# Optimization experiments

Hardware: AMD Instinct MI355X
Metric: run time of the kernel (lower is better)

The kernel has to match this reference:

```python
import jax, jax.numpy as jnp
import numpy as np

N_NODES = 50000
N_EDGES = 600000
IN_DIM, HID, OUT_DIM = 128, 128, 64
LN_EPS = 1e-5


def setup_inputs() -> dict:
    key = jax.random.key(0)
    ks = jax.random.split(key, 10)
    def glorot(k, shape):
        lim = np.sqrt(6.0 / (shape[0] + shape[1]))
        return jax.random.uniform(k, shape, jnp.float32, -lim, lim)
    return {
        "x": jax.random.normal(ks[0], (N_NODES, IN_DIM), jnp.float32),
        "src": jax.random.randint(ks[1], (N_EDGES,), 0, N_NODES, jnp.int32),
        "dst": jax.random.randint(ks[2], (N_EDGES,), 0, N_NODES, jnp.int32),
        "W0": glorot(ks[3], (IN_DIM, HID)), "b0": jnp.zeros((HID,), jnp.float32),
        "W1": glorot(ks[4], (HID, HID)),    "b1": jnp.zeros((HID,), jnp.float32),
        "W2": glorot(ks[5], (HID, OUT_DIM)),"b2": jnp.zeros((OUT_DIM,), jnp.float32),
        "ln_scale": jnp.ones((HID,), jnp.float32),
        "ln_bias": jnp.zeros((HID,), jnp.float32),
    }


def _degree_norms(src, dst):
    ones = jnp.ones((src.shape[0],), jnp.float32)
    deg_out = jax.ops.segment_sum(ones, src, num_segments=N_NODES)
    deg_in = jax.ops.segment_sum(ones, dst, num_segments=N_NODES)
    # DGL clamps degree to min 1 for norm='both'
    out_norm = jnp.clip(deg_out, 1.0, None) ** -0.5
    in_norm = jnp.clip(deg_in, 1.0, None) ** -0.5
    return out_norm, in_norm


def _graph_conv(h, src, dst, out_norm, in_norm, W, b):
    # norm='both': scale src side, SpMM aggregate, scale dst side, then affine
    h = h * out_norm[:, None]
    h = h @ W  # apply weight first (mathematically identical, smaller messages when out<in)
    agg = jax.ops.segment_sum(h[src], dst, num_segments=N_NODES)  # [N, D]
    return agg * in_norm[:, None] + b


def _layernorm(h, scale, bias):
    mu = jnp.mean(h, axis=-1, keepdims=True)
    var = jnp.var(h, axis=-1, keepdims=True)
    return (h - mu) * jax.lax.rsqrt(var + LN_EPS) * scale + bias


def reference(x, src, dst, W0, b0, W1, b1, W2, b2, ln_scale, ln_bias):
    out_norm, in_norm = _degree_norms(src, dst)
    # dropout is identity in eval mode
    h = jax.nn.relu(_graph_conv(x, src, dst, out_norm, in_norm, W0, b0))
    h = _layernorm(h, ln_scale, ln_bias)
    h = jax.nn.relu(_graph_conv(h, src, dst, out_norm, in_norm, W1, b1))
    h = _layernorm(h, ln_scale, ln_bias)
    # last layer: encoding=True -> keep activation; no norm after last layer
    h = jax.nn.relu(_graph_conv(h, src, dst, out_norm, in_norm, W2, b2))
    return h
```

## Files before the change

kernel.cpp:

```cpp
#include <hip/hip_runtime.h>
#include <hip/hip_fp16.h>

#define NN 50000
#define NE 600000
#define LN_EPS 1e-5f
#define SCAN_B 49
#define RANGES 8
#define RSZ 6250
#define CHUNKS 30
#define CSZ 20000

typedef __attribute__((ext_vector_type(8))) _Float16 half8;
typedef __attribute__((ext_vector_type(4))) float floatx4;

__device__ __align__(16) __half g_h0[NN * 128];
__device__ __align__(16) __half g_h1[NN * 128];
__device__ float g_out_norm[NN];
__device__ float g_in_norm[NN];
__device__ int g_rowptr[NN + 1];
__device__ int g_esrc[NE];
__device__ int g_blocksum[SCAN_B];
__device__ int g_perm[NN];
__device__ int g_dhist[SCAN_B * 256];
__device__ int g_pout[CHUNKS * NN];
__device__ int g_pin[CHUNKS * NN];
__device__ int g_base[CHUNKS * NN];
__device__ unsigned g_bar_count = 0;
__device__ unsigned g_bar_gen = 0;

__device__ __forceinline__ __half* hbuf(int i) { return i ? g_h1 : g_h0; }

__device__ __forceinline__ void gridbar(unsigned* expected) {
    __syncthreads();
    if (threadIdx.x == 0) {
        __threadfence();
        unsigned prev = __hip_atomic_fetch_add(&g_bar_count, 1u, __ATOMIC_ACQ_REL,
                                               __HIP_MEMORY_SCOPE_AGENT);
        if (prev == gridDim.x - 1) {
            __hip_atomic_store(&g_bar_count, 0u, __ATOMIC_RELAXED, __HIP_MEMORY_SCOPE_AGENT);
            __hip_atomic_fetch_add(&g_bar_gen, 1u, __ATOMIC_RELEASE, __HIP_MEMORY_SCOPE_AGENT);
        } else {
            while (__hip_atomic_load(&g_bar_gen, __ATOMIC_ACQUIRE, __HIP_MEMORY_SCOPE_AGENT) ==
                   *expected)
                __builtin_amdgcn_s_sleep(8);
        }
        __threadfence();
    }
    __syncthreads();
    (*expected)++;
}

__global__ __launch_bounds__(256) void histo_kernel(const int* __restrict__ src,
                                                    const int* __restrict__ dst) {
    __shared__ int h_out[RSZ];
    __shared__ int h_in[RSZ];
    int c = blockIdx.x / RANGES, r = blockIdx.x % RANGES;
    int lo = r * RSZ;
    for (int i = threadIdx.x; i < RSZ; i += 256) { h_out[i] = 0; h_in[i] = 0; }
    __syncthreads();
    const int4* s4 = (const int4*)(src + c * CSZ);
    const int4* d4 = (const int4*)(dst + c * CSZ);
    for (int i = threadIdx.x; i < CSZ / 4; i += 256) {
        int4 s = s4[i], d = d4[i];
        int v;
        v = s.x - lo; if ((unsigned)v < RSZ) atomicAdd(&h_out[v], 1);
        v = s.y - lo; if ((unsigned)v < RSZ) atomicAdd(&h_out[v], 1);
        v = s.z - lo; if ((unsigned)v < RSZ) atomicAdd(&h_out[v], 1);
        v = s.w - lo; if ((unsigned)v < RSZ) atomicAdd(&h_out[v], 1);
        v = d.x - lo; if ((unsigned)v < RSZ) atomicAdd(&h_in[v], 1);
        v = d.y - lo; if ((unsigned)v < RSZ) atomicAdd(&h_in[v], 1);
        v = d.z - lo; if ((unsigned)v < RSZ) atomicAdd(&h_in[v], 1);
        v = d.w - lo; if ((unsigned)v < RSZ) atomicAdd(&h_in[v], 1);
    }
    __syncthreads();
    for (int i = threadIdx.x; i < RSZ; i += 256) {
        g_pout[c * NN + lo + i] = h_out[i];
        g_pin[c * NN + lo + i]  = h_in[i];
    }
}

__global__ __launch_bounds__(1024) void mid_kernel() {
    __shared__ int sums[1024];
    __shared__ int aux[64];
    __shared__ int hist[256];
    __shared__ int cursor[256];
    unsigned expected = __hip_atomic_load(&g_bar_gen, __ATOMIC_RELAXED, __HIP_MEMORY_SCOPE_AGENT);
    int b = blockIdx.x, t = threadIdx.x;
    int n = b * 1024 + t;
    if (t < 256) hist[t] = 0;
    int si = 0;
    if (n < NN) {
        int so = 0;
#pragma unroll
        for (int c = 0; c < CHUNKS; ++c) { so += g_pout[c * NN + n]; si += g_pin[c * NN + n]; }
        g_out_norm[n] = rsqrtf((float)max(so, 1));
        g_in_norm[n]  = rsqrtf((float)max(si, 1));
    }
    __syncthreads();
    int bin = min(si, 255);
    if (n < NN) atomicAdd(&hist[bin], 1);
    int s = si;
#pragma unroll
    for (int off = 32; off; off >>= 1) s += __shfl_xor(s, off, 64);
    if ((t & 63) == 0) aux[t >> 6] = s;
    __syncthreads();
    if (t < 256) g_dhist[b * 256 + t] = hist[t];
    if (t < 16) {
        int v = aux[t];
#pragma unroll
        for (int off = 8; off; off >>= 1) v += __shfl_xor(v, off, 16);
        if (t == 0) g_blocksum[b] = v;
    }
    gridbar(&expected);
    if (t < 64) {
        int own = (t < SCAN_B) ? g_blocksum[t] : 0;
        int v = own;
#pragma unroll
        for (int off = 1; off < 64; off <<= 1) {
            int nb = __shfl_up(v, off, 64);
            if (t >= off) v += nb;
        }
        aux[t] = v - own;
        if (b == 0 && t == SCAN_B - 1) g_rowptr[NN] = v;
    }
    __syncthreads();
    int blockoff = aux[b];
    sums[t] = si;
    __syncthreads();
    for (int off = 1; off < 1024; off <<= 1) {
        int add = (t >= off) ? sums[t - off] : 0;
        __syncthreads();
        sums[t] += add;
        __syncthreads();
    }
    int excl = sums[t] - si + blockoff;
    if (n < NN) {
        g_rowptr[n] = excl;
        int run = excl;
#pragma unroll
        for (int c = 0; c < CHUNKS; ++c) {
            g_base[c * NN + n] = run;
            run += g_pin[c * NN + n];
        }
    }
    int cur = 0, tot = 0;
    if (t < 256) {
        for (int b2 = 0; b2 < SCAN_B; ++b2) {
            int h = g_dhist[b2 * 256 + t];
            if (b2 < b) cur += h;
            tot += h;
        }
        cursor[t] = tot;
    }
    __syncthreads();
    for (int off = 1; off < 256; off <<= 1) {
        int add = (t < 256 && t >= off) ? cursor[t - off] : 0;
        __syncthreads();
        if (t < 256) cursor[t] += add;
        __syncthreads();
    }
    if (t < 256) cursor[t] = cursor[t] - tot + cur;
    __syncthreads();
    if (n < NN) {
        int pos = atomicAdd(&cursor[bin], 1);
        g_perm[pos] = n;
    }
}

__global__ __launch_bounds__(256) void place_lds_kernel(const int* __restrict__ src,
                                                        const int* __restrict__ dst) {
    __shared__ int cur[RSZ];
    int c = blockIdx.x / RANGES, r = blockIdx.x % RANGES;
    int lo = r * RSZ;
    for (int i = threadIdx.x; i < RSZ; i += 256) cur[i] = g_base[c * NN + lo + i];
    __syncthreads();
    const int4* s4 = (const int4*)(src + c * CSZ);
    const int4* d4 = (const int4*)(dst + c * CSZ);
    for (int i = threadIdx.x; i < CSZ / 4; i += 256) {
        int4 s = s4[i], d = d4[i];
        int v, p;
        v = d.x - lo; if ((unsigned)v < RSZ) { p = atomicAdd(&cur[v], 1); g_esrc[p] = s.x; }
        v = d.y - lo; if ((unsigned)v < RSZ) { p = atomicAdd(&cur[v], 1); g_esrc[p] = s.y; }
        v = d.z - lo; if ((unsigned)v < RSZ) { p = atomicAdd(&cur[v], 1); g_esrc[p] = s.z; }
        v = d.w - lo; if ((unsigned)v < RSZ) { p = atomicAdd(&cur[v], 1); g_esrc[p] = s.w; }
    }
}

template <int N, bool AEXT>
__global__ __launch_bounds__(256) void gemm_mfma(const float* __restrict__ Aext,
                                                 int a_ib, int c_ib,
                                                 const float* __restrict__ Wg,
                                                 int M) {
    constexpr int NT = N / 16;
    constexpr int LOGN = (N == 128) ? 7 : 6;
    __shared__ _Float16 Wl[128 * N];

    const int tid = threadIdx.x;
    for (int e = tid; e < 128 * N; e += 256) {
        int k = e >> LOGN, n = e & (N - 1);
        Wl[(((k >> 3) * N + n) << 3) + (k & 7)] = (_Float16)Wg[e];
    }
    __syncthreads();

    const int wv = tid >> 6, lane = tid & 63;
    const int quad = lane >> 4, mrow = lane & 15;
    const int rowbase = blockIdx.x * 64 + wv * 16;
    const int arow0 = rowbase + mrow;
    const int arow = (arow0 < M) ? arow0 : (M - 1);

    floatx4 acc[NT] = {};
    const __half* Ah = AEXT ? nullptr : hbuf(a_ib);

#pragma unroll
    for (int kk = 0; kk < 4; ++kk) {
        const int k0 = kk * 32 + quad * 8;
        half8 afrag;
        if (AEXT) {
            const float4* ap = (const float4*)(Aext + (size_t)arow * 128 + k0);
            float4 f0 = ap[0], f1 = ap[1];
            afrag[0] = (_Float16)f0.x; afrag[1] = (_Float16)f0.y;
            afrag[2] = (_Float16)f0.z; afrag[3] = (_Float16)f0.w;
            afrag[4] = (_Float16)f1.x; afrag[5] = (_Float16)f1.y;
            afrag[6] = (_Float16)f1.z; afrag[7] = (_Float16)f1.w;
        } else {
            afrag = *(const half8*)(Ah + (size_t)arow * 128 + k0);
        }
#pragma unroll
        for (int nt = 0; nt < NT; ++nt) {
            half8 bfrag = *(const half8*)&Wl[(((kk * 4 + quad) * N + nt * 16 + mrow) << 3)];
            acc[nt] = __builtin_amdgcn_mfma_f32_16x16x32_f16(afrag, bfrag, acc[nt], 0, 0, 0);
        }
    }

    __half* C = hbuf(c_ib);
#pragma unroll
    for (int r = 0; r < 4; ++r) {
        int crow = rowbase + quad * 4 + r;
        if (crow < M) {
            float s = g_out_norm[crow];
#pragma unroll
            for (int nt = 0; nt < NT; ++nt) {
                float v = acc[nt][r] * s;
                C[(size_t)crow * N + nt * 16 + mrow] = __float2half_rn(v);
            }
        }
    }
}

#define ACC8(u) { \
    float2 f0 = __half22float2(*(const __half2*)&(u).x); \
    float2 f1 = __half22float2(*(const __half2*)&(u).y); \
    float2 f2 = __half22float2(*(const __half2*)&(u).z); \
    float2 f3 = __half22float2(*(const __half2*)&(u).w); \
    a0 += f0.x; a1 += f0.y; a2 += f1.x; a3 += f1.y; \
    a4 += f2.x; a5 += f2.y; a6 += f3.x; a7 += f3.y; }

__global__ __launch_bounds__(256) void gather_ln_kernel(int s_ib, int d_ib,
                                                        const float* __restrict__ b,
                                                        const float* __restrict__ ln_s,
                                                        const float* __restrict__ ln_b) {
    int wave = threadIdx.x >> 6;
    int lane = threadIdx.x & 63;
    int sub = lane >> 4, sl = lane & 15;
    int idx = blockIdx.x * 16 + wave * 4 + sub;
    int node = g_perm[idx];
    const uint4* Hu = (const uint4*)hbuf(s_ib);
    int beg = g_rowptr[node], end = g_rowptr[node + 1];
    float a0 = 0.f, a1 = 0.f, a2 = 0.f, a3 = 0.f, a4 = 0.f, a5 = 0.f, a6 = 0.f, a7 = 0.f;
    int j = beg;
    for (; j + 3 < end; j += 4) {
        int s0 = g_esrc[j], s1 = g_esrc[j + 1], s2 = g_esrc[j + 2], s3 = g_esrc[j + 3];
        uint4 u0 = Hu[s0 * 16 + sl];
        uint4 u1 = Hu[s1 * 16 + sl];
        uint4 u2 = Hu[s2 * 16 + sl];
        uint4 u3 = Hu[s3 * 16 + sl];
        ACC8(u0); ACC8(u1); ACC8(u2); ACC8(u3);
    }
    for (; j < end; ++j) {
        uint4 u = Hu[g_esrc[j] * 16 + sl];
        ACC8(u);
    }
    float nrm = g_in_norm[node];
    float4 bA = ((const float4*)b)[sl * 2], bB = ((const float4*)b)[sl * 2 + 1];
    float v0 = fmaxf(a0 * nrm + bA.x, 0.f), v1 = fmaxf(a1 * nrm + bA.y, 0.f);
    float v2 = fmaxf(a2 * nrm + bA.z, 0.f), v3 = fmaxf(a3 * nrm + bA.w, 0.f);
    float v4 = fmaxf(a4 * nrm + bB.x, 0.f), v5 = fmaxf(a5 * nrm + bB.y, 0.f);
    float v6 = fmaxf(a6 * nrm + bB.z, 0.f), v7 = fmaxf(a7 * nrm + bB.w, 0.f);
    float s = ((v0 + v1) + (v2 + v3)) + ((v4 + v5) + (v6 + v7));
    float sq = ((v0 * v0 + v1 * v1) + (v2 * v2 + v3 * v3)) +
               ((v4 * v4 + v5 * v5) + (v6 * v6 + v7 * v7));
#pragma unroll
    for (int off = 8; off > 0; off >>= 1) {
        s  += __shfl_xor(s, off, 64);
        sq += __shfl_xor(sq, off, 64);
    }
    float mean = s * (1.f / 128.f);
    float var = sq * (1.f / 128.f) - mean * mean;
    float inv = rsqrtf(var + LN_EPS);
    float4 lsA = ((const float4*)ln_s)[sl * 2], lsB = ((const float4*)ln_s)[sl * 2 + 1];
    float4 lbA = ((const float4*)ln_b)[sl * 2], lbB = ((const float4*)ln_b)[sl * 2 + 1];
    __half2 h0 = __floats2half2_rn((v0 - mean) * inv * lsA.x + lbA.x, (v1 - mean) * inv * lsA.y + lbA.y);
    __half2 h1 = __floats2half2_rn((v2 - mean) * inv * lsA.z + lbA.z, (v3 - mean) * inv * lsA.w + lbA.w);
    __half2 h2 = __floats2half2_rn((v4 - mean) * inv * lsB.x + lbB.x, (v5 - mean) * inv * lsB.y + lbB.y);
    __half2 h3 = __floats2half2_rn((v6 - mean) * inv * lsB.z + lbB.z, (v7 - mean) * inv * lsB.w + lbB.w);
    uint4 o = make_uint4(*(const unsigned int*)&h0, *(const unsigned int*)&h1,
                         *(const unsigned int*)&h2, *(const unsigned int*)&h3);
    ((uint4*)hbuf(d_ib))[node * 16 + sl] = o;
}

__global__ __launch_bounds__(256) void GCN_63831803953156_kernel(int s_ib,
                                                                 const float* __restrict__ b2,
                                                                 float* __restrict__ out) {
    int wave = threadIdx.x >> 6;
    int lane = threadIdx.x & 63;
    int sub = lane >> 3, sl = lane & 7;
    int idx = blockIdx.x * 32 + wave * 8 + sub;
    if (idx >= NN) return;
    int node = g_perm[idx];
    const uint4* Hu = (const uint4*)hbuf(s_ib);
    int beg = g_rowptr[node], end = g_rowptr[node + 1];
    float a0 = 0.f, a1 = 0.f, a2 = 0.f, a3 = 0.f, a4 = 0.f, a5 = 0.f, a6 = 0.f, a7 = 0.f;
    int j = beg;
    for (; j + 3 < end; j += 4) {
        int s0 = g_esrc[j], s1 = g_esrc[j + 1], s2 = g_esrc[j + 2], s3 = g_esrc[j + 3];
        uint4 u0 = Hu[s0 * 8 + sl];
        uint4 u1 = Hu[s1 * 8 + sl];
        uint4 u2 = Hu[s2 * 8 + sl];
        uint4 u3 = Hu[s3 * 8 + sl];
        ACC8(u0); ACC8(u1); ACC8(u2); ACC8(u3);
    }
    for (; j < end; ++j) {
        uint4 u = Hu[g_esrc[j] * 8 + sl];
        ACC8(u);
    }
    float nrm = g_in_norm[node];
    float4 bA = ((const float4*)b2)[sl * 2], bB = ((const float4*)b2)[sl * 2 + 1];
    float4 oA, oB;
    oA.x = fmaxf(a0 * nrm + bA.x, 0.f); oA.y = fmaxf(a1 * nrm + bA.y, 0.f);
    oA.z = fmaxf(a2 * nrm + bA.z, 0.f); oA.w = fmaxf(a3 * nrm + bA.w, 0.f);
    oB.x = fmaxf(a4 * nrm + bB.x, 0.f); oB.y = fmaxf(a5 * nrm + bB.y, 0.f);
    oB.z = fmaxf(a6 * nrm + bB.z, 0.f); oB.w = fmaxf(a7 * nrm + bB.w, 0.f);
    ((float4*)out)[node * 16 + sl * 2] = oA;
    ((float4*)out)[node * 16 + sl * 2 + 1] = oB;
}

extern "C" void kernel_launch(void* const* d_in, const int* in_sizes, int n_in,
                              void* d_out, int out_size, void* d_ws, size_t ws_size,
                              hipStream_t stream) {
    const float* x   = (const float*)d_in[0];
    const int* src   = (const int*)d_in[1];
    const int* dst   = (const int*)d_in[2];
    const float* W0  = (const float*)d_in[3];
    const float* b0  = (const float*)d_in[4];
    const float* W1  = (const float*)d_in[5];
    const float* b1  = (const float*)d_in[6];
    const float* W2  = (const float*)d_in[7];
    const float* b2  = (const float*)d_in[8];
    const float* ln_s = (const float*)d_in[9];
    const float* ln_b = (const float*)d_in[10];
    (void)d_ws; (void)ws_size; (void)in_sizes; (void)n_in; (void)out_size;

    histo_kernel<<<CHUNKS * RANGES, 256, 0, stream>>>(src, dst);
    mid_kernel<<<SCAN_B, 1024, 0, stream>>>();
    place_lds_kernel<<<CHUNKS * RANGES, 256, 0, stream>>>(src, dst);

    const int GB = (NN + 63) / 64;

    gemm_mfma<128, true><<<GB, 256, 0, stream>>>(x, -1, 0, W0, NN);
    gather_ln_kernel<<<NN / 16, 256, 0, stream>>>(0, 1, b0, ln_s, ln_b);

    gemm_mfma<128, false><<<GB, 256, 0, stream>>>(nullptr, 1, 0, W1, NN);
    gather_ln_kernel<<<NN / 16, 256, 0, stream>>>(0, 1, b1, ln_s, ln_b);

    gemm_mfma<64, false><<<GB, 256, 0, stream>>>(nullptr, 1, 0, W2, NN);
    GCN_63831803953156_kernel<<<(NN + 31) / 32, 256, 0, stream>>>(0, b2, (float*)d_out);
}
```

Measured before the change: 244.7 us.

## Fuse first GEMM into histogram kernel and apply out-norm during gather

The layer-0 GEMM (x @ W0) now runs as extra blocks inside the degree histogram kernel, so it no longer waits for the norms. The out_norm scaling is moved into the first gather as a per-edge weight. The mid kernel's LDS Hillis-Steele scans are replaced by wave shuffle scans, and the gather loops are unrolled by 8 to keep more loads in flight. The costs are an extra per-edge norm load in layer 0 and a mixed-role kernel whose block types differ in LDS use. The later layers still appear to rely on the gemm kernel epilogue for source-side scaling, which is not visible here.

```diff
diff --git a/kernel.cpp b/kernel.cpp
--- a/kernel.cpp
+++ b/kernel.cpp
@@ -9,6 +9,8 @@
 #define RSZ 6250
 #define CHUNKS 30
 #define CSZ 20000
+#define HB (CHUNKS * RANGES)
+#define GB ((NN + 63) / 64)
 
 typedef __attribute__((ext_vector_type(8))) _Float16 half8;
 typedef __attribute__((ext_vector_type(4))) float floatx4;
@@ -50,43 +52,91 @@
     (*expected)++;
 }
 
-__global__ __launch_bounds__(256) void histo_kernel(const int* __restrict__ src,
-                                                    const int* __restrict__ dst) {
-    __shared__ int h_out[RSZ];
-    __shared__ int h_in[RSZ];
-    int c = blockIdx.x / RANGES, r = blockIdx.x % RANGES;
-    int lo = r * RSZ;
-    for (int i = threadIdx.x; i < RSZ; i += 256) { h_out[i] = 0; h_in[i] = 0; }
-    __syncthreads();
-    const int4* s4 = (const int4*)(src + c * CSZ);
-    const int4* d4 = (const int4*)(dst + c * CSZ);
-    for (int i = threadIdx.x; i < CSZ / 4; i += 256) {
-        int4 s = s4[i], d = d4[i];
-        int v;
-        v = s.x - lo; if ((unsigned)v < RSZ) atomicAdd(&h_out[v], 1);
-        v = s.y - lo; if ((unsigned)v < RSZ) atomicAdd(&h_out[v], 1);
-        v = s.z - lo; if ((unsigned)v < RSZ) atomicAdd(&h_out[v], 1);
-        v = s.w - lo; if ((unsigned)v < RSZ) atomicAdd(&h_out[v], 1);
-        v = d.x - lo; if ((unsigned)v < RSZ) atomicAdd(&h_in[v], 1);
-        v = d.y - lo; if ((unsigned)v < RSZ) atomicAdd(&h_in[v], 1);
-        v = d.z - lo; if ((unsigned)v < RSZ) atomicAdd(&h_in[v], 1);
-        v = d.w - lo; if ((unsigned)v < RSZ) atomicAdd(&h_in[v], 1);
-    }
-    __syncthreads();
-    for (int i = threadIdx.x; i < RSZ; i += 256) {
-        g_pout[c * NN + lo + i] = h_out[i];
-        g_pin[c * NN + lo + i]  = h_in[i];
+__global__ __launch_bounds__(256) void k1_kernel(const int* __restrict__ src,
+                                                 const int* __restrict__ dst,
+                                                 const float* __restrict__ x,
+                                                 const float* __restrict__ W0) {
+    __shared__ __align__(16) int s_buf[2 * RSZ];
+    const int tid = threadIdx.x;
+    if (blockIdx.x < HB) {
+        int* h_out = s_buf;
+        int* h_in = s_buf + RSZ;
+        int c = blockIdx.x / RANGES, r = blockIdx.x % RANGES;
+        int lo = r * RSZ;
+        for (int i = tid; i < RSZ; i += 256) { h_out[i] = 0; h_in[i] = 0; }
+        __syncthreads();
+        const int4* s4 = (const int4*)(src + c * CSZ);
+        const int4* d4 = (const int4*)(dst + c * CSZ);
+        for (int i = tid; i < CSZ / 4; i += 256) {
+            int4 s = s4[i], d = d4[i];
+            int v;
+            v = s.x - lo; if ((unsigned)v < RSZ) atomicAdd(&h_out[v], 1);
+            v = s.y - lo; if ((unsigned)v < RSZ) atomicAdd(&h_out[v], 1);
+            v = s.z - lo; if ((unsigned)v < RSZ) atomicAdd(&h_out[v], 1);
+            v = s.w - lo; if ((unsigned)v < RSZ) atomicAdd(&h_out[v], 1);
+            v = d.x - lo; if ((unsigned)v < RSZ) atomicAdd(&h_in[v], 1);
+            v = d.y - lo; if ((unsigned)v < RSZ) atomicAdd(&h_in[v], 1);
+            v = d.z - lo; if ((unsigned)v < RSZ) atomicAdd(&h_in[v], 1);
+            v = d.w - lo; if ((unsigned)v < RSZ) atomicAdd(&h_in[v], 1);
+        }
+        __syncthreads();
+        for (int i = tid; i < RSZ; i += 256) {
+            g_pout[c * NN + lo + i] = h_out[i];
+            g_pin[c * NN + lo + i]  = h_in[i];
+        }
+    } else {
+        _Float16* Wl = (_Float16*)s_buf;
+        for (int e = tid; e < 128 * 128; e += 256) {
+            int k = e >> 7, n = e & 127;
+            Wl[(((k >> 3) * 128 + n) << 3) + (k & 7)] = (_Float16)W0[e];
+        }
+        __syncthreads();
+        const int gb = blockIdx.x - HB;
+        const int wv = tid >> 6, lane = tid & 63;
+        const int quad = lane >> 4, mrow = lane & 15;
+        const int rowbase = gb * 64 + wv * 16;
+        const int arow0 = rowbase + mrow;
+        const int arow = (arow0 < NN) ? arow0 : (NN - 1);
+        floatx4 acc[8] = {};
+#pragma unroll
+        for (int kk = 0; kk < 4; ++kk) {
+            const int k0 = kk * 32 + quad * 8;
+            const float4* ap = (const float4*)(x + (size_t)arow * 128 + k0);
+            float4 f0 = ap[0], f1 = ap[1];
+            half8 afrag;
+            afrag[0] = (_Float16)f0.x; afrag[1] = (_Float16)f0.y;
+            afrag[2] = (_Float16)f0.z; afrag[3] = (_Float16)f0.w;
+            afrag[4] = (_Float16)f1.x; afrag[5] = (_Float16)f1.y;
+            afrag[6] = (_Float16)f1.z; afrag[7] = (_Float16)f1.w;
+#pragma unroll
+            for (int nt = 0; nt < 8; ++nt) {
+                half8 bfrag = *(const half8*)&Wl[(((kk * 4 + quad) * 128 + nt * 16 + mrow) << 3)];
+                acc[nt] = __builtin_amdgcn_mfma_f32_16x16x32_f16(afrag, bfrag, acc[nt], 0, 0, 0);
+            }
+        }
+        __half* C = hbuf(0);
+#pragma unroll
+        for (int r = 0; r < 4; ++r) {
+            int crow = rowbase + quad * 4 + r;
+            if (crow < NN) {
+#pragma unroll
+                for (int nt = 0; nt < 8; ++nt)
+                    C[(size_t)crow * 128 + nt * 16 + mrow] = __float2half_rn(acc[nt][r]);
+            }
+        }
     }
 }
 
 __global__ __launch_bounds__(1024) void mid_kernel() {
-    __shared__ int sums[1024];
-    __shared__ int aux[64];
+    __shared__ int wsum[16], woff[16];
+    __shared__ int bscan[64];
     __shared__ int hist[256];
     __shared__ int cursor[256];
+    __shared__ int cwsum[4], cwoff[4];
     unsigned expected = __hip_atomic_load(&g_bar_gen, __ATOMIC_RELAXED, __HIP_MEMORY_SCOPE_AGENT);
-    int b = blockIdx.x, t = threadIdx.x;
-    int n = b * 1024 + t;
+    const int b = blockIdx.x, t = threadIdx.x;
+    const int lane = t & 63, wv = t >> 6;
+    const int n = b * 1024 + t;
     if (t < 256) hist[t] = 0;
     int si = 0;
     if (n < NN) {
@@ -99,17 +149,24 @@
     __syncthreads();
     int bin = min(si, 255);
     if (n < NN) atomicAdd(&hist[bin], 1);
-    int s = si;
-#pragma unroll
-    for (int off = 32; off; off >>= 1) s += __shfl_xor(s, off, 64);
-    if ((t & 63) == 0) aux[t >> 6] = s;
+    int inc = si;
+#pragma unroll
+    for (int off = 1; off < 64; off <<= 1) {
+        int p = __shfl_up(inc, off, 64);
+        if (lane >= off) inc += p;
+    }
+    if (lane == 63) wsum[wv] = inc;
     __syncthreads();
     if (t < 256) g_dhist[b * 256 + t] = hist[t];
     if (t < 16) {
-        int v = aux[t];
-#pragma unroll
-        for (int off = 8; off; off >>= 1) v += __shfl_xor(v, off, 16);
-        if (t == 0) g_blocksum[b] = v;
+        int x = wsum[t], y = x;
+#pragma unroll
+        for (int off = 1; off < 16; off <<= 1) {
+            int p = __shfl_up(y, off, 16);
+            if (t >= off) y += p;
+        }
+        woff[t] = y - x;
+        if (t == 15) g_blocksum[b] = y;
     }
     gridbar(&expected);
     if (t < 64) {
@@ -117,23 +174,14 @@
         int v = own;
 #pragma unroll
         for (int off = 1; off < 64; off <<= 1) {
-            int nb = __shfl_up(v, off, 64);
-            if (t >= off) v += nb;
-        }
-        aux[t] = v - own;
+            int p = __shfl_up(v, off, 64);
+            if (t >= off) v += p;
+        }
+        bscan[t] = v - own;
         if (b == 0 && t == SCAN_B - 1) g_rowptr[NN] = v;
     }
     __syncthreads();
-    int blockoff = aux[b];
-    sums[t] = si;
-    __syncthreads();
-    for (int off = 1; off < 1024; off <<= 1) {
-        int add = (t >= off) ? sums[t - off] : 0;
-        __syncthreads();
-        sums[t] += add;
-        __syncthreads();
-    }
-    int excl = sums[t] - si + blockoff;
+    int excl = (inc - si) + woff[wv] + bscan[b];
     if (n < NN) {
         g_rowptr[n] = excl;
         int run = excl;
@@ -147,19 +195,29 @@
     if (t < 256) {
         for (int b2 = 0; b2 < SCAN_B; ++b2) {
             int h = g_dhist[b2 * 256 + t];
-            if (b2 < b) cur += h;
+            cur += (b2 < b) ? h : 0;
             tot += h;
         }
-        cursor[t] = tot;
-    }
-    __syncthreads();
-    for (int off = 1; off < 256; off <<= 1) {
-        int add = (t < 256 && t >= off) ? cursor[t - off] : 0;
-        __syncthreads();
-        if (t < 256) cursor[t] += add;
-        __syncthreads();
-    }
-    if (t < 256) cursor[t] = cursor[t] - tot + cur;
+    }
+    int cinc = tot;
+#pragma unroll
+    for (int off = 1; off < 64; off <<= 1) {
+        int p = __shfl_up(cinc, off, 64);
+        if (lane >= off) cinc += p;
+    }
+    if (t < 256 && lane == 63) cwsum[wv] = cinc;
+    __syncthreads();
+    if (t < 4) {
+        int x = cwsum[t], y = x;
+#pragma unroll
+        for (int off = 1; off < 4; off <<= 1) {
+            int p = __shfl_up(y, off, 4);
+            if (t >= off) y += p;
+        }
+        cwoff[t] = y - x;
+    }
+    __syncthreads();
+    if (t < 256) cursor[t] = (cinc - tot) + cwoff[wv] + cur;
     __syncthreads();
     if (n < NN) {
         int pos = atomicAdd(&cursor[bin], 1);
@@ -186,11 +244,9 @@
     }
 }
 
-template <int N, bool AEXT>
-__global__ __launch_bounds__(256) void gemm_mfma(const float* __restrict__ Aext,
-                                                 int a_ib, int c_ib,
-                                                 const float* __restrict__ Wg,
-                                                 int M) {
+template <int N>
+__global__ __launch_bounds__(256) void gemm_mfma(int a_ib, int c_ib,
+                                                 const float* __restrict__ Wg, int M) {
     constexpr int NT = N / 16;
     constexpr int LOGN = (N == 128) ? 7 : 6;
     __shared__ _Float16 Wl[128 * N];
@@ -209,22 +265,12 @@
     const int arow = (arow0 < M) ? arow0 : (M - 1);
 
     floatx4 acc[NT] = {};
-    const __half* Ah = AEXT ? nullptr : hbuf(a_ib);
+    const __half* Ah = hbuf(a_ib);
 
 #pragma unroll
     for (int kk = 0; kk < 4; ++kk) {
         const int k0 = kk * 32 + quad * 8;
-        half8 afrag;
-        if (AEXT) {
-            const float4* ap = (const float4*)(Aext + (size_t)arow * 128 + k0);
-            float4 f0 = ap[0], f1 = ap[1];
-            afrag[0] = (_Float16)f0.x; afrag[1] = (_Float16)f0.y;
-            afrag[2] = (_Float16)f0.z; afrag[3] = (_Float16)f0.w;
-            afrag[4] = (_Float16)f1.x; afrag[5] = (_Float16)f1.y;
-            afrag[6] = (_Float16)f1.z; afrag[7] = (_Float16)f1.w;
-        } else {
-            afrag = *(const half8*)(Ah + (size_t)arow * 128 + k0);
-        }
+        half8 afrag = *(const half8*)(Ah + (size_t)arow * 128 + k0);
 #pragma unroll
         for (int nt = 0; nt < NT; ++nt) {
             half8 bfrag = *(const half8*)&Wl[(((kk * 4 + quad) * N + nt * 16 + mrow) << 3)];
@@ -247,14 +293,20 @@
     }
 }
 
-#define ACC8(u) { \
-    float2 f0 = __half22float2(*(const __half2*)&(u).x); \
-    float2 f1 = __half22float2(*(const __half2*)&(u).y); \
-    float2 f2 = __half22float2(*(const __half2*)&(u).z); \
-    float2 f3 = __half22float2(*(const __half2*)&(u).w); \
-    a0 += f0.x; a1 += f0.y; a2 += f1.x; a3 += f1.y; \
-    a4 += f2.x; a5 += f2.y; a6 += f3.x; a7 += f3.y; }
-
+__device__ __forceinline__ void acc_row(uint4 u, float wt,
+                                        float& a0, float& a1, float& a2, float& a3,
+                                        float& a4, float& a5, float& a6, float& a7) {
+    float2 f0 = __half22float2(*(const __half2*)&u.x);
+    float2 f1 = __half22float2(*(const __half2*)&u.y);
+    float2 f2 = __half22float2(*(const __half2*)&u.z);
+    float2 f3 = __half22float2(*(const __half2*)&u.w);
+    a0 = fmaf(wt, f0.x, a0); a1 = fmaf(wt, f0.y, a1);
+    a2 = fmaf(wt, f1.x, a2); a3 = fmaf(wt, f1.y, a3);
+    a4 = fmaf(wt, f2.x, a4); a5 = fmaf(wt, f2.y, a5);
+    a6 = fmaf(wt, f3.x, a6); a7 = fmaf(wt, f3.y, a7);
+}
+
+template <bool SC>
 __global__ __launch_bounds__(256) void gather_ln_kernel(int s_ib, int d_ib,
                                                         const float* __restrict__ b,
                                                         const float* __restrict__ ln_s,
@@ -268,17 +320,32 @@
     int beg = g_rowptr[node], end = g_rowptr[node + 1];
     float a0 = 0.f, a1 = 0.f, a2 = 0.f, a3 = 0.f, a4 = 0.f, a5 = 0.f, a6 = 0.f, a7 = 0.f;
     int j = beg;
+    for (; j + 7 < end; j += 8) {
+        int ss[8]; uint4 uu[8]; float ww[8];
+#pragma unroll
+        for (int q = 0; q < 8; ++q) ss[q] = g_esrc[j + q];
+#pragma unroll
+        for (int q = 0; q < 8; ++q) uu[q] = Hu[ss[q] * 16 + sl];
+#pragma unroll
+        for (int q = 0; q < 8; ++q) ww[q] = SC ? g_out_norm[ss[q]] : 1.0f;
+#pragma unroll
+        for (int q = 0; q < 8; ++q) acc_row(uu[q], ww[q], a0, a1, a2, a3, a4, a5, a6, a7);
+    }
     for (; j + 3 < end; j += 4) {
-        int s0 = g_esrc[j], s1 = g_esrc[j + 1], s2 = g_esrc[j + 2], s3 = g_esrc[j + 3];
-        uint4 u0 = Hu[s0 * 16 + sl];
-        uint4 u1 = Hu[s1 * 16 + sl];
-        uint4 u2 = Hu[s2 * 16 + sl];
-        uint4 u3 = Hu[s3 * 16 + sl];
-        ACC8(u0); ACC8(u1); ACC8(u2); ACC8(u3);
+        int ss[4]; uint4 uu[4]; float ww[4];
+#pragma unroll
+        for (int q = 0; q < 4; ++q) ss[q] = g_esrc[j + q];
+#pragma unroll
+        for (int q = 0; q < 4; ++q) uu[q] = Hu[ss[q] * 16 + sl];
+#pragma unroll
+        for (int q = 0; q < 4; ++q) ww[q] = SC ? g_out_norm[ss[q]] : 1.0f;
+#pragma unroll
+        for (int q = 0; q < 4; ++q) acc_row(uu[q], ww[q], a0, a1, a2, a3, a4, a5, a6, a7);
     }
     for (; j < end; ++j) {
-        uint4 u = Hu[g_esrc[j] * 16 + sl];
-        ACC8(u);
+        int s0 = g_esrc[j];
+        float w0 = SC ? g_out_norm[s0] : 1.0f;
+        acc_row(Hu[s0 * 16 + sl], w0, a0, a1, a2, a3, a4, a5, a6, a7);
     }
     float nrm = g_in_norm[node];
     float4 bA = ((const float4*)b)[sl * 2], bB = ((const float4*)b)[sl * 2 + 1];
@@ -321,18 +388,26 @@
     int beg = g_rowptr[node], end = g_rowptr[node + 1];
     float a0 = 0.f, a1 = 0.f, a2 = 0.f, a3 = 0.f, a4 = 0.f, a5 = 0.f, a6 = 0.f, a7 = 0.f;
     int j = beg;
+    for (; j + 7 < end; j += 8) {
+        int ss[8]; uint4 uu[8];
+#pragma unroll
+        for (int q = 0; q < 8; ++q) ss[q] = g_esrc[j + q];
+#pragma unroll
+        for (int q = 0; q < 8; ++q) uu[q] = Hu[ss[q] * 8 + sl];
+#pragma unroll
+        for (int q = 0; q < 8; ++q) acc_row(uu[q], 1.0f, a0, a1, a2, a3, a4, a5, a6, a7);
+    }
     for (; j + 3 < end; j += 4) {
-        int s0 = g_esrc[j], s1 = g_esrc[j + 1], s2 = g_esrc[j + 2], s3 = g_esrc[j + 3];
-        uint4 u0 = Hu[s0 * 8 + sl];
-        uint4 u1 = Hu[s1 * 8 + sl];
-        uint4 u2 = Hu[s2 * 8 + sl];
-        uint4 u3 = Hu[s3 * 8 + sl];
-        ACC8(u0); ACC8(u1); ACC8(u2); ACC8(u3);
-    }
-    for (; j < end; ++j) {
-        uint4 u = Hu[g_esrc[j] * 8 + sl];
-        ACC8(u);
-    }
+        int ss[4]; uint4 uu[4];
+#pragma unroll
+        for (int q = 0; q < 4; ++q) ss[q] = g_esrc[j + q];
+#pragma unroll
+        for (int q = 0; q < 4; ++q) uu[q] = Hu[ss[q] * 8 + sl];
+#pragma unroll
+        for (int q = 0; q < 4; ++q) acc_row(uu[q], 1.0f, a0, a1, a2, a3, a4, a5, a6, a7);
+    }
+    for (; j < end; ++j)
+        acc_row(Hu[g_esrc[j] * 8 + sl], 1.0f, a0, a1, a2, a3, a4, a5, a6, a7);
     float nrm = g_in_norm[node];
     float4 bA = ((const float4*)b2)[sl * 2], bB = ((const float4*)b2)[sl * 2 + 1];
     float4 oA, oB;
@@ -360,18 +435,15 @@
     const float* ln_b = (const float*)d_in[10];
     (void)d_ws; (void)ws_size; (void)in_sizes; (void)n_in; (void)out_size;
 
-    histo_kernel<<<CHUNKS * RANGES, 256, 0, stream>>>(src, dst);
+    k1_kernel<<<HB + GB, 256, 0, stream>>>(src, dst, x, W0);
     mid_kernel<<<SCAN_B, 1024, 0, stream>>>();
-    place_lds_kernel<<<CHUNKS * RANGES, 256, 0, stream>>>(src, dst);
-
-    const int GB = (NN + 63) / 64;
-
-    gemm_mfma<128, true><<<GB, 256, 0, stream>>>(x, -1, 0, W0, NN);
-    gather_ln_kernel<<<NN / 16, 256, 0, stream>>>(0, 1, b0, ln_s, ln_b);
-
-    gemm_mfma<128, false><<<GB, 256, 0, stream>>>(nullptr, 1, 0, W1, NN);
-    gather_ln_kernel<<<NN / 16, 256, 0, stream>>>(0, 1, b1, ln_s, ln_b);
-
-    gemm_mfma<64, false><<<GB, 256, 0, stream>>>(nullptr, 1, 0, W2, NN);
+    place_lds_kernel<<<HB, 256, 0, stream>>>(src, dst);
+
+    gather_ln_kernel<true><<<NN / 16, 256, 0, stream>>>(0, 1, b0, ln_s, ln_b);
+
+    gemm_mfma<128><<<GB, 256, 0, stream>>>(1, 0, W1, NN);
+    gather_ln_kernel<false><<<NN / 16, 256, 0, stream>>>(0, 1, b1, ln_s, ln_b);
+
+    gemm_mfma<64><<<GB, 256, 0, stream>>>(1, 0, W2, NN);
     GCN_63831803953156_kernel<<<(NN + 31) / 32, 256, 0, stream>>>(0, b2, (float*)d_out);
 }
```

Measured after the change: 231.0 us, median of 2. -5.6%, faster.
